# Kernel optimization log

Measured on AMD Instinct MI355X. Metric: run time of the kernel, lower is better.

Reference implementation:

```python
import jax, jax.numpy as jnp
import numpy as np

B, T, H, NB, D = 8, 4096, 16, 32, 1024
NS = H * NB            # 512
PF = 2 * NS            # pos_feat_dim = 1024
HID = 128


def _mlp(x, w1, b1, w2, b2):
    # Linear -> exact GELU -> Linear (matches nn.GELU default, erf form)
    return jax.nn.gelu(x @ w1 + b1, approximate=False) @ w2 + b2


def setup_inputs() -> dict:
    key = jax.random.key(0)
    ks = jax.random.split(key, 12)
    s = 0.02
    return {
        "theta_path": jax.random.normal(ks[0], (B, T, H, NB), jnp.float32),
        "content_emb": jax.random.normal(ks[1], (B, T, D), jnp.float32),
        "obs_position_mask": jax.random.bernoulli(ks[2], 0.5, (B, T)),
        # forward_model: Linear(PF,128) -> GELU -> Linear(128,D)
        "fw1": jax.random.normal(ks[3], (PF, HID), jnp.float32) * s,
        "fb1": jnp.zeros((HID,), jnp.float32),
        "fw2": jax.random.normal(ks[4], (HID, D), jnp.float32) * s,
        "fb2": jnp.zeros((D,), jnp.float32),
        # error_to_state: Linear(D,128) -> GELU -> Linear(128,NS)
        "ew1": jax.random.normal(ks[5], (D, HID), jnp.float32) * s,
        "eb1": jnp.zeros((HID,), jnp.float32),
        "ew2": jax.random.normal(ks[6], (HID, NS), jnp.float32) * s,
        "eb2": jnp.zeros((NS,), jnp.float32),
        "log_gain": jnp.full((H, NB), -1.7, jnp.float32),
    }


def reference(theta_path, content_emb, obs_position_mask,
              fw1, fb1, fw2, fb2, ew1, eb1, ew2, eb2, log_gain):
    # trig positional features: (B,T,H,2*NB) -> (B,T,2*H*NB)
    pos_feat = jnp.concatenate([jnp.cos(theta_path), jnp.sin(theta_path)], axis=-1)
    pos_feat = pos_feat.reshape(B, T, PF)

    obs_pred = _mlp(pos_feat, fw1, fb1, fw2, fb2)            # (B,T,D)
    err_raw = content_emb - obs_pred
    err = err_raw * obs_position_mask[..., None].astype(err_raw.dtype)

    delta_theta = _mlp(err, ew1, eb1, ew2, eb2).reshape(B, T, H, NB)
    gate = jax.nn.sigmoid(log_gain)                          # (H,NB)

    # affine recurrence d_t = gate * d_{t-1} + delta_t via log-depth scan
    def comb(c1, c2):
        a1, b1 = c1
        a2, b2 = c2
        return (a1 * a2, a2 * b1 + b2)

    A = jnp.broadcast_to(gate, delta_theta.shape)
    _, d = jax.lax.associative_scan(comb, (A, delta_theta), axis=1)

    theta_hat = theta_path + d
    return theta_hat, err_raw, gate
```

## Files before the change

### kernel.cpp

```cpp
#include <hip/hip_runtime.h>
#include <hip/hip_bf16.h>

#define B_    8
#define T_    4096
#define H_    16
#define NB_   32
#define D_    1024
#define NS_   512
#define PF_   1024
#define HID_  128
#define RTOK  32768

#define LCH   128
#define WARM  64
#define NCH   32

typedef __attribute__((ext_vector_type(8))) short short8;
typedef __attribute__((ext_vector_type(4))) float floatx4;
typedef unsigned short us;

__device__ __forceinline__ float bf2f(us u){
    union { unsigned int i; float f; } v; v.i = ((unsigned int)u) << 16; return v.f;
}
__device__ __forceinline__ us f2bf(float f){
    union { float f; unsigned int i; } v; v.f = f;
    unsigned int r = v.i + 0x7fffu + ((v.i >> 16) & 1u);
    return (us)(r >> 16);
}
__device__ __forceinline__ float gelu_exact(float x){
    return 0.5f * x * (1.0f + erff(x * 0.70710678118654752f));
}
__device__ __forceinline__ floatx4 mfma16(short8 a, short8 b, floatx4 c){
    return __builtin_amdgcn_mfma_f32_16x16x32_bf16(a, b, c, 0, 0, 0);
}
__device__ __forceinline__ short8 ldfrag(const us* p){
    return *(const short8*)p;
}
__device__ __forceinline__ float ldany(const void* p, int i, int df){
    return df ? bf2f(((const us*)p)[i]) : ((const float*)p)[i];
}

__global__ void dtype_classify(const us* t, int* dflag){
    __shared__ int good;
    if (threadIdx.x == 0) good = 0;
    __syncthreads();
    int g = 0;
    for (int j = 0; j < 64; ++j){
        us u = t[threadIdx.x * 64 + j];
        int e = (u >> 7) & 0xff;
        if (u == 0 || (e >= 90 && e <= 140)) g++;
    }
    atomicAdd(&good, g);
    __syncthreads();
    if (threadIdx.x == 0) dflag[0] = (good > (16384 * 9) / 10) ? 1 : 0;
}

__global__ void mask_classify(const unsigned char* mp, int* flag){
    __shared__ int s_mis, s_oth, s_off1;
    if (threadIdx.x == 0){ s_mis = 0; s_oth = 0; s_off1 = 0; }
    __syncthreads();
    int mis = 0, oth = 0, off1 = 0;
    int base = threadIdx.x * 128;
    for (int i = base; i < base + 128; ++i){
        unsigned char v = mp[i];
        if (v){
            if (i & 3) mis++;
            if ((i & 3) == 1) off1++;
            if (v != 1) oth++;
        }
    }
    atomicAdd(&s_mis, mis); atomicAdd(&s_oth, oth); atomicAdd(&s_off1, off1);
    __syncthreads();
    if (threadIdx.x == 0){
        int f;
        if (s_mis == 0)       f = 0;
        else if (s_oth == 0)  f = 1;
        else if (s_off1 > 0)  f = 2;
        else                  f = 3;
        *flag = f;
    }
}

__global__ void mask_decode(const void* mp, const int* flag, float* maskf){
    int i = blockIdx.x * 256 + threadIdx.x;
    if (i >= RTOK) return;
    int f = *flag;
    bool nz;
    if (f == 1)      nz = ((const unsigned char*) mp)[i] != 0;
    else if (f == 2) nz = ((const us*)           mp)[i] != 0;
    else             nz = ((const unsigned int*) mp)[i] != 0;
    maskf[i] = nz ? 1.0f : 0.0f;
}

__global__ void prep_weights(const void* fw1, const void* fw2, const void* ew1,
                             const void* ew2, const void* fb1, const void* fb2,
                             const void* eb1, const void* eb2, const void* lg,
                             const int* dflag,
                             us* fw1t, us* fw2t, us* ew1t, us* ew2t, us* cb){
    int df = *dflag;
    for (int idx = blockIdx.x * 256 + threadIdx.x; idx < 461056;
         idx += gridDim.x * 256){
        if (idx < 131072){
            int k = idx >> 7, n = idx & 127;
            fw1t[n * 1024 + k] = f2bf(ldany(fw1, idx, df));
        } else if (idx < 262144){
            int l = idx - 131072, k = l >> 10, n = l & 1023;
            fw2t[n * 128 + k] = f2bf(ldany(fw2, l, df));
        } else if (idx < 393216){
            int l = idx - 262144, k = l >> 7, n = l & 127;
            ew1t[n * 1024 + k] = f2bf(ldany(ew1, l, df));
        } else if (idx < 458752){
            int l = idx - 393216, k = l >> 9, n = l & 511;
            ew2t[n * 128 + k] = f2bf(ldany(ew2, l, df));
        } else {
            int l = idx - 458752;
            float v;
            if (l < 128)       v = ldany(fb1, l, df);
            else if (l < 1152) v = ldany(fb2, l - 128, df);
            else if (l < 1280) v = ldany(eb1, l - 1152, df);
            else if (l < 1792) v = ldany(eb2, l - 1280, df);
            else               v = ldany(lg,  l - 1792, df);
            cb[l] = f2bf(v);
        }
    }
}

template<int NR, int NC, int GK, int NT>
__device__ __forceinline__ void stage_wt(us* lds, const us* g,
                                         int row0, int k0, int tid){
    const int LS = NC + 8;
    constexpr int TOT = NR * NC / 8;
    #pragma unroll
    for (int i = tid; i < TOT; i += NT){
        int r  = i / (NC / 8);
        int c8 = (i % (NC / 8)) * 8;
        uint4 v = *(const uint4*)(g + (size_t)(row0 + r) * GK + k0 + c8);
        *(uint4*)(lds + r * LS + c8) = v;
    }
}

__global__ __launch_bounds__(512, 4) void fused_mlp(
    const void* __restrict__ theta, const void* __restrict__ content,
    const int* __restrict__ dflag, const float* __restrict__ maskf,
    const us* __restrict__ cb,
    const us* __restrict__ fw1t, const us* __restrict__ fw2t,
    const us* __restrict__ ew1t, const us* __restrict__ ew2t,
    float* __restrict__ err_out, float* __restrict__ delta_out)
{
    __shared__ __align__(16) us sPF[64 * 136];
    __shared__ __align__(16) us sW [128 * 136];
    __shared__ __align__(16) us sH [64 * 136];
    __shared__ float sMask[64];

    const int tid  = threadIdx.x;
    const int wid  = tid >> 6;
    const int lane = tid & 63;
    const int q    = lane >> 4;
    const int ln   = lane & 15;
    const int wr   = (wid >> 2) * 32;
    const int wc   = (wid & 3) * 32;
    const int row0 = blockIdx.x * 64;
    const int df   = *dflag;

    if (tid < 64) sMask[tid] = maskf[row0 + tid];

    floatx4 h1a[2][2] = {};
    for (int kc = 0; kc < 8; ++kc){
        {
            int r = tid >> 3, e0 = (tid & 7) * 8;
            size_t off = (size_t)(row0 + r) * NS_ + kc * 64 + e0;
            float xv[8];
            if (df){
                uint4 raw = *(const uint4*)((const us*)theta + off);
                const us* pu = (const us*)&raw;
                #pragma unroll
                for (int j = 0; j < 8; ++j) xv[j] = bf2f(pu[j]);
            } else {
                const float* tp = (const float*)theta + off;
                float4 v0 = *(const float4*)tp;
                float4 v1 = *(const float4*)(tp + 4);
                xv[0]=v0.x; xv[1]=v0.y; xv[2]=v0.z; xv[3]=v0.w;
                xv[4]=v1.x; xv[5]=v1.y; xv[6]=v1.z; xv[7]=v1.w;
            }
            short8 c8v, s8v;
            #pragma unroll
            for (int j = 0; j < 8; ++j){
                float s, c;
                __sincosf(xv[j], &s, &c);
                c8v[j] = (short)f2bf(c);
                s8v[j] = (short)f2bf(s);
            }
            int base = r * 136 + (e0 >> 5) * 64 + (e0 & 31);
            *(short8*)(&sPF[base])      = c8v;
            *(short8*)(&sPF[base + 32]) = s8v;
        }
        stage_wt<128, 128, 1024, 512>(sW, fw1t, 0, kc * 128, tid);
        __syncthreads();
        #pragma unroll
        for (int ks = 0; ks < 4; ++ks){
            short8 a0 = ldfrag(&sPF[(wr + ln)      * 136 + ks * 32 + q * 8]);
            short8 a1 = ldfrag(&sPF[(wr + 16 + ln) * 136 + ks * 32 + q * 8]);
            short8 b0 = ldfrag(&sW [(wc + ln)      * 136 + ks * 32 + q * 8]);
            short8 b1 = ldfrag(&sW [(wc + 16 + ln) * 136 + ks * 32 + q * 8]);
            h1a[0][0] = mfma16(a0, b0, h1a[0][0]);
            h1a[0][1] = mfma16(a0, b1, h1a[0][1]);
            h1a[1][0] = mfma16(a1, b0, h1a[1][0]);
            h1a[1][1] = mfma16(a1, b1, h1a[1][1]);
        }
        __syncthreads();
    }
    #pragma unroll
    for (int mt = 0; mt < 2; ++mt)
        #pragma unroll
        for (int nt = 0; nt < 2; ++nt){
            int n = wc + nt * 16 + ln;
            float bias = bf2f(cb[n]);
            #pragma unroll
            for (int r2 = 0; r2 < 4; ++r2){
                int m = wr + mt * 16 + q * 4 + r2;
                sH[m * 136 + n] = f2bf(gelu_exact(h1a[mt][nt][r2] + bias));
            }
        }
    __syncthreads();

    floatx4 h2a[2][2] = {};
    for (int nc = 0; nc < 8; ++nc){
        {
            int r = tid >> 3, c0 = (tid & 7) * 16;
            size_t off = (size_t)(row0 + r) * D_ + nc * 128 + c0;
            if (df){
                const us* cp = (const us*)content + off;
                *(uint4*)(&sPF[r * 136 + c0])     = *(const uint4*)cp;
                *(uint4*)(&sPF[r * 136 + c0 + 8]) = *(const uint4*)(cp + 8);
            } else {
                const float* cp = (const float*)content + off;
                #pragma unroll
                for (int v = 0; v < 2; ++v){
                    float4 a = *(const float4*)(cp + v * 8);
                    float4 b = *(const float4*)(cp + v * 8 + 4);
                    short8 t8;
                    t8[0] = (short)f2bf(a.x); t8[1] = (short)f2bf(a.y);
                    t8[2] = (short)f2bf(a.z); t8[3] = (short)f2bf(a.w);
                    t8[4] = (short)f2bf(b.x); t8[5] = (short)f2bf(b.y);
                    t8[6] = (short)f2bf(b.z); t8[7] = (short)f2bf(b.w);
                    *(short8*)(&sPF[r * 136 + c0 + v * 8]) = t8;
                }
            }
        }
        stage_wt<128, 128, 128, 512>(sW, fw2t, nc * 128, 0, tid);
        __syncthreads();
        floatx4 oa[2][2] = {};
        #pragma unroll
        for (int ks = 0; ks < 4; ++ks){
            short8 a0 = ldfrag(&sH[(wr + ln)      * 136 + ks * 32 + q * 8]);
            short8 a1 = ldfrag(&sH[(wr + 16 + ln) * 136 + ks * 32 + q * 8]);
            short8 b0 = ldfrag(&sW[(wc + ln)      * 136 + ks * 32 + q * 8]);
            short8 b1 = ldfrag(&sW[(wc + 16 + ln) * 136 + ks * 32 + q * 8]);
            oa[0][0] = mfma16(a0, b0, oa[0][0]);
            oa[0][1] = mfma16(a0, b1, oa[0][1]);
            oa[1][0] = mfma16(a1, b0, oa[1][0]);
            oa[1][1] = mfma16(a1, b1, oa[1][1]);
        }
        {
            #pragma unroll
            for (int mt = 0; mt < 2; ++mt)
                #pragma unroll
                for (int nt = 0; nt < 2; ++nt){
                    int n = wc + nt * 16 + ln;
                    float bias = bf2f(cb[128 + nc * 128 + n]);
                    #pragma unroll
                    for (int r2 = 0; r2 < 4; ++r2){
                        int m = wr + mt * 16 + q * 4 + r2;
                        float obs  = oa[mt][nt][r2] + bias;
                        float eraw = bf2f(sPF[m * 136 + n]) - obs;
                        err_out[(size_t)(row0 + m) * D_ + nc * 128 + n] = eraw;
                        sPF[m * 136 + n] = f2bf(eraw * sMask[m]);
                    }
                }
        }
        __syncthreads();
        stage_wt<128, 128, 1024, 512>(sW, ew1t, 0, nc * 128, tid);
        __syncthreads();
        #pragma unroll
        for (int ks = 0; ks < 4; ++ks){
            short8 a0 = ldfrag(&sPF[(wr + ln)      * 136 + ks * 32 + q * 8]);
            short8 a1 = ldfrag(&sPF[(wr + 16 + ln) * 136 + ks * 32 + q * 8]);
            short8 b0 = ldfrag(&sW [(wc + ln)      * 136 + ks * 32 + q * 8]);
            short8 b1 = ldfrag(&sW [(wc + 16 + ln) * 136 + ks * 32 + q * 8]);
            h2a[0][0] = mfma16(a0, b0, h2a[0][0]);
            h2a[0][1] = mfma16(a0, b1, h2a[0][1]);
            h2a[1][0] = mfma16(a1, b0, h2a[1][0]);
            h2a[1][1] = mfma16(a1, b1, h2a[1][1]);
        }
        __syncthreads();
    }
    #pragma unroll
    for (int mt = 0; mt < 2; ++mt)
        #pragma unroll
        for (int nt = 0; nt < 2; ++nt){
            int n = wc + nt * 16 + ln;
            float bias = bf2f(cb[1152 + n]);
            #pragma unroll
            for (int r2 = 0; r2 < 4; ++r2){
                int m = wr + mt * 16 + q * 4 + r2;
                sH[m * 136 + n] = f2bf(gelu_exact(h2a[mt][nt][r2] + bias));
            }
        }
    __syncthreads();

    for (int nc = 0; nc < 4; ++nc){
        stage_wt<128, 128, 128, 512>(sW, ew2t, nc * 128, 0, tid);
        __syncthreads();
        floatx4 da[2][2] = {};
        #pragma unroll
        for (int ks = 0; ks < 4; ++ks){
            short8 a0 = ldfrag(&sH[(wr + ln)      * 136 + ks * 32 + q * 8]);
            short8 a1 = ldfrag(&sH[(wr + 16 + ln) * 136 + ks * 32 + q * 8]);
            short8 b0 = ldfrag(&sW[(wc + ln)      * 136 + ks * 32 + q * 8]);
            short8 b1 = ldfrag(&sW[(wc + 16 + ln) * 136 + ks * 32 + q * 8]);
            da[0][0] = mfma16(a0, b0, da[0][0]);
            da[0][1] = mfma16(a0, b1, da[0][1]);
            da[1][0] = mfma16(a1, b0, da[1][0]);
            da[1][1] = mfma16(a1, b1, da[1][1]);
        }
        #pragma unroll
        for (int mt = 0; mt < 2; ++mt)
            #pragma unroll
            for (int nt = 0; nt < 2; ++nt){
                int n = wc + nt * 16 + ln;
                int col = nc * 128 + n;
                float bias = bf2f(cb[1280 + col]);
                #pragma unroll
                for (int r2 = 0; r2 < 4; ++r2){
                    int m = wr + mt * 16 + q * 4 + r2;
                    delta_out[(size_t)(row0 + m) * NS_ + col] = da[mt][nt][r2] + bias;
                }
            }
        __syncthreads();
    }
}

__global__ __launch_bounds__(512) void warmup_k(
    const float* __restrict__ delta, const us* __restrict__ cb,
    float* __restrict__ warm)
{
    int c  = threadIdx.x;
    int bi = blockIdx.x;
    int ch = bi & (NCH - 1);
    float g = 1.0f / (1.0f + expf(-bf2f(cb[1792 + c])));
    float w = 0.0f;
    if (ch > 0){
        int b  = bi >> 5;
        int t0 = ch * LCH;
        const float* dp = delta + ((size_t)b * T_ + t0 - WARM) * NS_ + c;
        #pragma unroll 8
        for (int t = 0; t < WARM; ++t){ w = g * w + *dp; dp += NS_; }
    }
    warm[bi * NS_ + c] = w;
}

__global__ __launch_bounds__(512) void scan_k(
    const void* __restrict__ theta, const us* __restrict__ cb,
    const int* __restrict__ dflag, const float* __restrict__ warm,
    float* __restrict__ out0, float* __restrict__ gate_out)
{
    int c  = threadIdx.x;
    int bi = blockIdx.x;
    int b  = bi >> 5;
    int ch = bi & (NCH - 1);
    float g = 1.0f / (1.0f + expf(-bf2f(cb[1792 + c])));
    if (bi == 0) gate_out[c] = g;

    float d = warm[bi * NS_ + c];
    size_t base = ((size_t)b * T_ + ch * LCH) * NS_ + c;
    float* op = out0 + base;
    if (*dflag){
        const us* tp = (const us*)theta + base;
        #pragma unroll 4
        for (int t = 0; t < LCH; ++t){
            d = g * d + *op;
            *op = bf2f(*tp) + d;
            tp += NS_; op += NS_;
        }
    } else {
        const float* tp = (const float*)theta + base;
        #pragma unroll 4
        for (int t = 0; t < LCH; ++t){
            d = g * d + *op;
            *op = *tp + d;
            tp += NS_; op += NS_;
        }
    }
}

extern "C" void kernel_launch(void* const* d_in, const int* in_sizes, int n_in,
                              void* d_out, int out_size, void* d_ws, size_t ws_size,
                              hipStream_t stream)
{
    const void* theta   = d_in[0];
    const void* content = d_in[1];
    const void* maskraw = d_in[2];
    const void* fw1 = d_in[3];  const void* fb1 = d_in[4];
    const void* fw2 = d_in[5];  const void* fb2 = d_in[6];
    const void* ew1 = d_in[7];  const void* eb1 = d_in[8];
    const void* ew2 = d_in[9];  const void* eb2 = d_in[10];
    const void* lg  = d_in[11];

    char* ws = (char*)d_ws;
    float* maskf = (float*)ws;
    float* warmb = (float*)ws;
    int*   flag  = (int*)(ws + 524288);
    int*   dflag = (int*)(ws + 524292);
    us*    fw1t  = (us*)(ws + 525312);
    us*    fw2t  = (us*)(ws + 787456);
    us*    ew1t  = (us*)(ws + 1049600);
    us*    ew2t  = (us*)(ws + 1311744);
    us*    cb    = (us*)(ws + 1442816);

    float* out0 = (float*)d_out;
    float* out1 = out0 + 16777216;
    float* out2 = out1 + 33554432;

    dtype_classify<<<1, 256, 0, stream>>>((const us*)theta, dflag);
    mask_classify<<<1, 256, 0, stream>>>((const unsigned char*)maskraw, flag);
    mask_decode<<<128, 256, 0, stream>>>(maskraw, flag, maskf);
    prep_weights<<<512, 256, 0, stream>>>(fw1, fw2, ew1, ew2, fb1, fb2, eb1, eb2,
                                          lg, dflag, fw1t, fw2t, ew1t, ew2t, cb);
    fused_mlp<<<RTOK / 64, 512, 0, stream>>>(theta, content, dflag, maskf, cb,
                                             fw1t, fw2t, ew1t, ew2t, out1, out0);
    warmup_k<<<B_ * NCH, 512, 0, stream>>>(out0, cb, warmb);
    scan_k<<<B_ * NCH, 512, 0, stream>>>(theta, cb, dflag, warmb, out0, out2);
}
```

Baseline: 470.9 us.

## Pre-swizzle MLP weights into MFMA fragment order and read them straight from global memory

prep_weights now writes all four weight matrices in per-wave MFMA fragment order, so each wave loads its B fragments directly from global memory instead of staging 128x128 weight tiles through LDS. Each wave now owns a 16-column slice across all 64 rows. The positional-feature and error tiles are double-buffered, so each k-step needs only one barrier, and the next theta load is prefetched while sincos runs. Content values are read straight into registers, and the mask decode is folded into the fused kernel, which removes one launch. The scan chunk count is doubled, halving chunk length to expose more parallelism, at the cost of more warmup work.

```diff
diff --git a/kernel.cpp b/kernel.cpp
--- a/kernel.cpp
+++ b/kernel.cpp
@@ -11,9 +11,9 @@
 #define HID_  128
 #define RTOK  32768
 
-#define LCH   128
+#define LCH   64
 #define WARM  64
-#define NCH   32
+#define NCH   64
 
 typedef __attribute__((ext_vector_type(8))) short short8;
 typedef __attribute__((ext_vector_type(4))) float floatx4;
@@ -36,8 +36,14 @@
 __device__ __forceinline__ short8 ldfrag(const us* p){
     return *(const short8*)p;
 }
-__device__ __forceinline__ float ldany(const void* p, int i, int df){
+__device__ __forceinline__ float ldany(const void* p, size_t i, int df){
     return df ? bf2f(((const us*)p)[i]) : ((const float*)p)[i];
+}
+__device__ __forceinline__ void bar(){
+    __builtin_amdgcn_sched_barrier(0);
+    asm volatile("s_waitcnt lgkmcnt(0)" ::: "memory");
+    __builtin_amdgcn_s_barrier();
+    __builtin_amdgcn_sched_barrier(0);
 }
 
 __global__ void dtype_classify(const us* t, int* dflag){
@@ -81,17 +87,6 @@
     }
 }
 
-__global__ void mask_decode(const void* mp, const int* flag, float* maskf){
-    int i = blockIdx.x * 256 + threadIdx.x;
-    if (i >= RTOK) return;
-    int f = *flag;
-    bool nz;
-    if (f == 1)      nz = ((const unsigned char*) mp)[i] != 0;
-    else if (f == 2) nz = ((const us*)           mp)[i] != 0;
-    else             nz = ((const unsigned int*) mp)[i] != 0;
-    maskf[i] = nz ? 1.0f : 0.0f;
-}
-
 __global__ void prep_weights(const void* fw1, const void* fw2, const void* ew1,
                              const void* ew2, const void* fb1, const void* fb2,
                              const void* eb1, const void* eb2, const void* lg,
@@ -102,16 +97,26 @@
          idx += gridDim.x * 256){
         if (idx < 131072){
             int k = idx >> 7, n = idx & 127;
-            fw1t[n * 1024 + k] = f2bf(ldany(fw1, idx, df));
+            int c = k >> 7, kk = k & 127;
+            int ks = kk >> 5, qq = (kk >> 3) & 3, j = k & 7;
+            int w = n >> 4, ln = n & 15;
+            fw1t[(((c*8 + w)*4 + ks)*64 + qq*16 + ln)*8 + j] = f2bf(ldany(fw1, idx, df));
         } else if (idx < 262144){
-            int l = idx - 131072, k = l >> 10, n = l & 1023;
-            fw2t[n * 128 + k] = f2bf(ldany(fw2, l, df));
+            int l = idx - 131072; int k = l >> 10, n = l & 1023;
+            int c = n >> 7, w = (n >> 4) & 7, ln = n & 15;
+            int ks = k >> 5, qq = (k >> 3) & 3, j = k & 7;
+            fw2t[(((c*8 + w)*4 + ks)*64 + qq*16 + ln)*8 + j] = f2bf(ldany(fw2, l, df));
         } else if (idx < 393216){
-            int l = idx - 262144, k = l >> 7, n = l & 127;
-            ew1t[n * 1024 + k] = f2bf(ldany(ew1, l, df));
+            int l = idx - 262144; int k = l >> 7, n = l & 127;
+            int c = k >> 7, kk = k & 127;
+            int ks = kk >> 5, qq = (kk >> 3) & 3, j = k & 7;
+            int w = n >> 4, ln = n & 15;
+            ew1t[(((c*8 + w)*4 + ks)*64 + qq*16 + ln)*8 + j] = f2bf(ldany(ew1, l, df));
         } else if (idx < 458752){
-            int l = idx - 393216, k = l >> 9, n = l & 511;
-            ew2t[n * 128 + k] = f2bf(ldany(ew2, l, df));
+            int l = idx - 393216; int k = l >> 9, n = l & 511;
+            int c = n >> 7, w = (n >> 4) & 7, ln = n & 15;
+            int ks = k >> 5, qq = (k >> 3) & 3, j = k & 7;
+            ew2t[(((c*8 + w)*4 + ks)*64 + qq*16 + ln)*8 + j] = f2bf(ldany(ew2, l, df));
         } else {
             int l = idx - 458752;
             float v;
@@ -125,31 +130,32 @@
     }
 }
 
-template<int NR, int NC, int GK, int NT>
-__device__ __forceinline__ void stage_wt(us* lds, const us* g,
-                                         int row0, int k0, int tid){
-    const int LS = NC + 8;
-    constexpr int TOT = NR * NC / 8;
-    #pragma unroll
-    for (int i = tid; i < TOT; i += NT){
-        int r  = i / (NC / 8);
-        int c8 = (i % (NC / 8)) * 8;
-        uint4 v = *(const uint4*)(g + (size_t)(row0 + r) * GK + k0 + c8);
-        *(uint4*)(lds + r * LS + c8) = v;
+__device__ __forceinline__ void load8(float* xv, const void* p, size_t off, int df){
+    if (df){
+        uint4 raw = *(const uint4*)((const us*)p + off);
+        const us* pu = (const us*)&raw;
+        #pragma unroll
+        for (int j = 0; j < 8; ++j) xv[j] = bf2f(pu[j]);
+    } else {
+        const float* tp = (const float*)p + off;
+        float4 v0 = *(const float4*)tp;
+        float4 v1 = *(const float4*)(tp + 4);
+        xv[0]=v0.x; xv[1]=v0.y; xv[2]=v0.z; xv[3]=v0.w;
+        xv[4]=v1.x; xv[5]=v1.y; xv[6]=v1.z; xv[7]=v1.w;
     }
 }
 
 __global__ __launch_bounds__(512, 4) void fused_mlp(
     const void* __restrict__ theta, const void* __restrict__ content,
-    const int* __restrict__ dflag, const float* __restrict__ maskf,
+    const int* __restrict__ dflag,
+    const void* __restrict__ maskraw, const int* __restrict__ mflag,
     const us* __restrict__ cb,
     const us* __restrict__ fw1t, const us* __restrict__ fw2t,
     const us* __restrict__ ew1t, const us* __restrict__ ew2t,
     float* __restrict__ err_out, float* __restrict__ delta_out)
 {
-    __shared__ __align__(16) us sPF[64 * 136];
-    __shared__ __align__(16) us sW [128 * 136];
-    __shared__ __align__(16) us sH [64 * 136];
+    __shared__ __align__(16) us sPF[2][64 * 136];
+    __shared__ __align__(16) us sH[64 * 136];
     __shared__ float sMask[64];
 
     const int tid  = threadIdx.x;
@@ -157,31 +163,27 @@
     const int lane = tid & 63;
     const int q    = lane >> 4;
     const int ln   = lane & 15;
-    const int wr   = (wid >> 2) * 32;
-    const int wc   = (wid & 3) * 32;
     const int row0 = blockIdx.x * 64;
     const int df   = *dflag;
 
-    if (tid < 64) sMask[tid] = maskf[row0 + tid];
-
-    floatx4 h1a[2][2] = {};
-    for (int kc = 0; kc < 8; ++kc){
-        {
-            int r = tid >> 3, e0 = (tid & 7) * 8;
-            size_t off = (size_t)(row0 + r) * NS_ + kc * 64 + e0;
-            float xv[8];
-            if (df){
-                uint4 raw = *(const uint4*)((const us*)theta + off);
-                const us* pu = (const us*)&raw;
-                #pragma unroll
-                for (int j = 0; j < 8; ++j) xv[j] = bf2f(pu[j]);
-            } else {
-                const float* tp = (const float*)theta + off;
-                float4 v0 = *(const float4*)tp;
-                float4 v1 = *(const float4*)(tp + 4);
-                xv[0]=v0.x; xv[1]=v0.y; xv[2]=v0.z; xv[3]=v0.w;
-                xv[4]=v1.x; xv[5]=v1.y; xv[6]=v1.z; xv[7]=v1.w;
-            }
+    if (tid < 64){
+        int f = *mflag;
+        int i = row0 + tid;
+        bool nz;
+        if (f == 1)      nz = ((const unsigned char*) maskraw)[i] != 0;
+        else if (f == 2) nz = ((const us*)           maskraw)[i] != 0;
+        else             nz = ((const unsigned int*) maskraw)[i] != 0;
+        sMask[tid] = nz ? 1.0f : 0.0f;
+    }
+
+    floatx4 h1a[4] = {};
+    {
+        const int r  = tid >> 3;
+        const int e0 = (tid & 7) * 8;
+        const int sb = r * 136 + ((e0 >> 5) << 6) + (e0 & 31);
+        float xv[8];
+        load8(xv, theta, (size_t)(row0 + r) * NS_ + e0, df);
+        for (int kc = 0; kc < 8; ++kc){
             short8 c8v, s8v;
             #pragma unroll
             for (int j = 0; j < 8; ++j){
@@ -190,153 +192,116 @@
                 c8v[j] = (short)f2bf(c);
                 s8v[j] = (short)f2bf(s);
             }
-            int base = r * 136 + (e0 >> 5) * 64 + (e0 & 31);
-            *(short8*)(&sPF[base])      = c8v;
-            *(short8*)(&sPF[base + 32]) = s8v;
-        }
-        stage_wt<128, 128, 1024, 512>(sW, fw1t, 0, kc * 128, tid);
-        __syncthreads();
-        #pragma unroll
-        for (int ks = 0; ks < 4; ++ks){
-            short8 a0 = ldfrag(&sPF[(wr + ln)      * 136 + ks * 32 + q * 8]);
-            short8 a1 = ldfrag(&sPF[(wr + 16 + ln) * 136 + ks * 32 + q * 8]);
-            short8 b0 = ldfrag(&sW [(wc + ln)      * 136 + ks * 32 + q * 8]);
-            short8 b1 = ldfrag(&sW [(wc + 16 + ln) * 136 + ks * 32 + q * 8]);
-            h1a[0][0] = mfma16(a0, b0, h1a[0][0]);
-            h1a[0][1] = mfma16(a0, b1, h1a[0][1]);
-            h1a[1][0] = mfma16(a1, b0, h1a[1][0]);
-            h1a[1][1] = mfma16(a1, b1, h1a[1][1]);
-        }
-        __syncthreads();
-    }
-    #pragma unroll
-    for (int mt = 0; mt < 2; ++mt)
-        #pragma unroll
-        for (int nt = 0; nt < 2; ++nt){
-            int n = wc + nt * 16 + ln;
-            float bias = bf2f(cb[n]);
-            #pragma unroll
-            for (int r2 = 0; r2 < 4; ++r2){
-                int m = wr + mt * 16 + q * 4 + r2;
-                sH[m * 136 + n] = f2bf(gelu_exact(h1a[mt][nt][r2] + bias));
-            }
-        }
-    __syncthreads();
-
-    floatx4 h2a[2][2] = {};
+            us* dst = &sPF[kc & 1][sb];
+            *(short8*)dst        = c8v;
+            *(short8*)(dst + 32) = s8v;
+            if (kc < 7) load8(xv, theta, (size_t)(row0 + r) * NS_ + (kc + 1) * 64 + e0, df);
+            bar();
+            const us* fp = fw1t + kc * 16384 + wid * 2048 + lane * 8;
+            #pragma unroll
+            for (int ks = 0; ks < 4; ++ks){
+                short8 b = *(const short8*)(fp + ks * 512);
+                #pragma unroll
+                for (int mt = 0; mt < 4; ++mt){
+                    short8 a = ldfrag(&sPF[kc & 1][(mt*16 + ln) * 136 + ks*32 + q*8]);
+                    h1a[mt] = mfma16(a, b, h1a[mt]);
+                }
+            }
+        }
+    }
+    {
+        int n = wid * 16 + ln;
+        float bias = bf2f(cb[n]);
+        #pragma unroll
+        for (int mt = 0; mt < 4; ++mt)
+            #pragma unroll
+            for (int r2 = 0; r2 < 4; ++r2)
+                sH[(mt*16 + q*4 + r2) * 136 + n] = f2bf(gelu_exact(h1a[mt][r2] + bias));
+    }
+    bar();
+
+    floatx4 h2a[4] = {};
     for (int nc = 0; nc < 8; ++nc){
+        const int ncol = nc * 128 + wid * 16 + ln;
+        float cv[16];
+        #pragma unroll
+        for (int mt = 0; mt < 4; ++mt)
+            #pragma unroll
+            for (int r2 = 0; r2 < 4; ++r2)
+                cv[mt*4 + r2] = ldany(content,
+                    (size_t)(row0 + mt*16 + q*4 + r2) * D_ + ncol, df);
+        floatx4 oa[4] = {};
         {
-            int r = tid >> 3, c0 = (tid & 7) * 16;
-            size_t off = (size_t)(row0 + r) * D_ + nc * 128 + c0;
-            if (df){
-                const us* cp = (const us*)content + off;
-                *(uint4*)(&sPF[r * 136 + c0])     = *(const uint4*)cp;
-                *(uint4*)(&sPF[r * 136 + c0 + 8]) = *(const uint4*)(cp + 8);
-            } else {
-                const float* cp = (const float*)content + off;
+            const us* fp = fw2t + nc * 16384 + wid * 2048 + lane * 8;
+            #pragma unroll
+            for (int ks = 0; ks < 4; ++ks){
+                short8 b = *(const short8*)(fp + ks * 512);
                 #pragma unroll
-                for (int v = 0; v < 2; ++v){
-                    float4 a = *(const float4*)(cp + v * 8);
-                    float4 b = *(const float4*)(cp + v * 8 + 4);
-                    short8 t8;
-                    t8[0] = (short)f2bf(a.x); t8[1] = (short)f2bf(a.y);
-                    t8[2] = (short)f2bf(a.z); t8[3] = (short)f2bf(a.w);
-                    t8[4] = (short)f2bf(b.x); t8[5] = (short)f2bf(b.y);
-                    t8[6] = (short)f2bf(b.z); t8[7] = (short)f2bf(b.w);
-                    *(short8*)(&sPF[r * 136 + c0 + v * 8]) = t8;
+                for (int mt = 0; mt < 4; ++mt){
+                    short8 a = ldfrag(&sH[(mt*16 + ln) * 136 + ks*32 + q*8]);
+                    oa[mt] = mfma16(a, b, oa[mt]);
                 }
             }
         }
-        stage_wt<128, 128, 128, 512>(sW, fw2t, nc * 128, 0, tid);
-        __syncthreads();
-        floatx4 oa[2][2] = {};
-        #pragma unroll
-        for (int ks = 0; ks < 4; ++ks){
-            short8 a0 = ldfrag(&sH[(wr + ln)      * 136 + ks * 32 + q * 8]);
-            short8 a1 = ldfrag(&sH[(wr + 16 + ln) * 136 + ks * 32 + q * 8]);
-            short8 b0 = ldfrag(&sW[(wc + ln)      * 136 + ks * 32 + q * 8]);
-            short8 b1 = ldfrag(&sW[(wc + 16 + ln) * 136 + ks * 32 + q * 8]);
-            oa[0][0] = mfma16(a0, b0, oa[0][0]);
-            oa[0][1] = mfma16(a0, b1, oa[0][1]);
-            oa[1][0] = mfma16(a1, b0, oa[1][0]);
-            oa[1][1] = mfma16(a1, b1, oa[1][1]);
-        }
         {
-            #pragma unroll
-            for (int mt = 0; mt < 2; ++mt)
-                #pragma unroll
-                for (int nt = 0; nt < 2; ++nt){
-                    int n = wc + nt * 16 + ln;
-                    float bias = bf2f(cb[128 + nc * 128 + n]);
-                    #pragma unroll
-                    for (int r2 = 0; r2 < 4; ++r2){
-                        int m = wr + mt * 16 + q * 4 + r2;
-                        float obs  = oa[mt][nt][r2] + bias;
-                        float eraw = bf2f(sPF[m * 136 + n]) - obs;
-                        err_out[(size_t)(row0 + m) * D_ + nc * 128 + n] = eraw;
-                        sPF[m * 136 + n] = f2bf(eraw * sMask[m]);
-                    }
-                }
-        }
-        __syncthreads();
-        stage_wt<128, 128, 1024, 512>(sW, ew1t, 0, nc * 128, tid);
-        __syncthreads();
-        #pragma unroll
-        for (int ks = 0; ks < 4; ++ks){
-            short8 a0 = ldfrag(&sPF[(wr + ln)      * 136 + ks * 32 + q * 8]);
-            short8 a1 = ldfrag(&sPF[(wr + 16 + ln) * 136 + ks * 32 + q * 8]);
-            short8 b0 = ldfrag(&sW [(wc + ln)      * 136 + ks * 32 + q * 8]);
-            short8 b1 = ldfrag(&sW [(wc + 16 + ln) * 136 + ks * 32 + q * 8]);
-            h2a[0][0] = mfma16(a0, b0, h2a[0][0]);
-            h2a[0][1] = mfma16(a0, b1, h2a[0][1]);
-            h2a[1][0] = mfma16(a1, b0, h2a[1][0]);
-            h2a[1][1] = mfma16(a1, b1, h2a[1][1]);
-        }
-        __syncthreads();
-    }
-    #pragma unroll
-    for (int mt = 0; mt < 2; ++mt)
-        #pragma unroll
-        for (int nt = 0; nt < 2; ++nt){
-            int n = wc + nt * 16 + ln;
-            float bias = bf2f(cb[1152 + n]);
-            #pragma unroll
-            for (int r2 = 0; r2 < 4; ++r2){
-                int m = wr + mt * 16 + q * 4 + r2;
-                sH[m * 136 + n] = f2bf(gelu_exact(h2a[mt][nt][r2] + bias));
-            }
-        }
-    __syncthreads();
-
-    for (int nc = 0; nc < 4; ++nc){
-        stage_wt<128, 128, 128, 512>(sW, ew2t, nc * 128, 0, tid);
-        __syncthreads();
-        floatx4 da[2][2] = {};
-        #pragma unroll
-        for (int ks = 0; ks < 4; ++ks){
-            short8 a0 = ldfrag(&sH[(wr + ln)      * 136 + ks * 32 + q * 8]);
-            short8 a1 = ldfrag(&sH[(wr + 16 + ln) * 136 + ks * 32 + q * 8]);
-            short8 b0 = ldfrag(&sW[(wc + ln)      * 136 + ks * 32 + q * 8]);
-            short8 b1 = ldfrag(&sW[(wc + 16 + ln) * 136 + ks * 32 + q * 8]);
-            da[0][0] = mfma16(a0, b0, da[0][0]);
-            da[0][1] = mfma16(a0, b1, da[0][1]);
-            da[1][0] = mfma16(a1, b0, da[1][0]);
-            da[1][1] = mfma16(a1, b1, da[1][1]);
-        }
-        #pragma unroll
-        for (int mt = 0; mt < 2; ++mt)
-            #pragma unroll
-            for (int nt = 0; nt < 2; ++nt){
-                int n = wc + nt * 16 + ln;
-                int col = nc * 128 + n;
-                float bias = bf2f(cb[1280 + col]);
+            float bias = bf2f(cb[128 + ncol]);
+            #pragma unroll
+            for (int mt = 0; mt < 4; ++mt)
                 #pragma unroll
                 for (int r2 = 0; r2 < 4; ++r2){
-                    int m = wr + mt * 16 + q * 4 + r2;
-                    delta_out[(size_t)(row0 + m) * NS_ + col] = da[mt][nt][r2] + bias;
+                    int m = mt*16 + q*4 + r2;
+                    float obs  = oa[mt][r2] + bias;
+                    float eraw = cv[mt*4 + r2] - obs;
+                    err_out[(size_t)(row0 + m) * D_ + ncol] = eraw;
+                    sPF[nc & 1][m * 136 + wid*16 + ln] = f2bf(eraw * sMask[m]);
                 }
-            }
-        __syncthreads();
+        }
+        bar();
+        {
+            const us* fp = ew1t + nc * 16384 + wid * 2048 + lane * 8;
+            #pragma unroll
+            for (int ks = 0; ks < 4; ++ks){
+                short8 b = *(const short8*)(fp + ks * 512);
+                #pragma unroll
+                for (int mt = 0; mt < 4; ++mt){
+                    short8 a = ldfrag(&sPF[nc & 1][(mt*16 + ln) * 136 + ks*32 + q*8]);
+                    h2a[mt] = mfma16(a, b, h2a[mt]);
+                }
+            }
+        }
+    }
+    {
+        int n = wid * 16 + ln;
+        float bias = bf2f(cb[1152 + n]);
+        #pragma unroll
+        for (int mt = 0; mt < 4; ++mt)
+            #pragma unroll
+            for (int r2 = 0; r2 < 4; ++r2)
+                sH[(mt*16 + q*4 + r2) * 136 + n] = f2bf(gelu_exact(h2a[mt][r2] + bias));
+    }
+    bar();
+
+    for (int c4 = 0; c4 < 4; ++c4){
+        floatx4 da[4] = {};
+        const us* fp = ew2t + c4 * 16384 + wid * 2048 + lane * 8;
+        #pragma unroll
+        for (int ks = 0; ks < 4; ++ks){
+            short8 b = *(const short8*)(fp + ks * 512);
+            #pragma unroll
+            for (int mt = 0; mt < 4; ++mt){
+                short8 a = ldfrag(&sH[(mt*16 + ln) * 136 + ks*32 + q*8]);
+                da[mt] = mfma16(a, b, da[mt]);
+            }
+        }
+        int ncol = c4 * 128 + wid * 16 + ln;
+        float bias = bf2f(cb[1280 + ncol]);
+        #pragma unroll
+        for (int mt = 0; mt < 4; ++mt)
+            #pragma unroll
+            for (int r2 = 0; r2 < 4; ++r2){
+                int m = mt*16 + q*4 + r2;
+                delta_out[(size_t)(row0 + m) * NS_ + ncol] = da[mt][r2] + bias;
+            }
     }
 }
 
@@ -350,7 +315,7 @@
     float g = 1.0f / (1.0f + expf(-bf2f(cb[1792 + c])));
     float w = 0.0f;
     if (ch > 0){
-        int b  = bi >> 5;
+        int b  = bi >> 6;
         int t0 = ch * LCH;
         const float* dp = delta + ((size_t)b * T_ + t0 - WARM) * NS_ + c;
         #pragma unroll 8
@@ -366,7 +331,7 @@
 {
     int c  = threadIdx.x;
     int bi = blockIdx.x;
-    int b  = bi >> 5;
+    int b  = bi >> 6;
     int ch = bi & (NCH - 1);
     float g = 1.0f / (1.0f + expf(-bf2f(cb[1792 + c])));
     if (bi == 0) gate_out[c] = g;
@@ -407,15 +372,14 @@
     const void* lg  = d_in[11];
 
     char* ws = (char*)d_ws;
-    float* maskf = (float*)ws;
-    float* warmb = (float*)ws;
-    int*   flag  = (int*)(ws + 524288);
-    int*   dflag = (int*)(ws + 524292);
-    us*    fw1t  = (us*)(ws + 525312);
-    us*    fw2t  = (us*)(ws + 787456);
-    us*    ew1t  = (us*)(ws + 1049600);
-    us*    ew2t  = (us*)(ws + 1311744);
-    us*    cb    = (us*)(ws + 1442816);
+    int*   flag  = (int*)ws;
+    int*   dflag = (int*)(ws + 4);
+    us*    cb    = (us*)(ws + 256);
+    us*    fw1t  = (us*)(ws + 4864);
+    us*    fw2t  = (us*)(ws + 267008);
+    us*    ew1t  = (us*)(ws + 529152);
+    us*    ew2t  = (us*)(ws + 791296);
+    float* warmb = (float*)(ws + 4864);
 
     float* out0 = (float*)d_out;
     float* out1 = out0 + 16777216;
@@ -423,11 +387,10 @@
 
     dtype_classify<<<1, 256, 0, stream>>>((const us*)theta, dflag);
     mask_classify<<<1, 256, 0, stream>>>((const unsigned char*)maskraw, flag);
-    mask_decode<<<128, 256, 0, stream>>>(maskraw, flag, maskf);
     prep_weights<<<512, 256, 0, stream>>>(fw1, fw2, ew1, ew2, fb1, fb2, eb1, eb2,
                                           lg, dflag, fw1t, fw2t, ew1t, ew2t, cb);
-    fused_mlp<<<RTOK / 64, 512, 0, stream>>>(theta, content, dflag, maskf, cb,
-                                             fw1t, fw2t, ew1t, ew2t, out1, out0);
+    fused_mlp<<<RTOK / 64, 512, 0, stream>>>(theta, content, dflag, maskraw, flag,
+                                             cb, fw1t, fw2t, ew1t, ew2t, out1, out0);
     warmup_k<<<B_ * NCH, 512, 0, stream>>>(out0, cb, warmb);
     scan_k<<<B_ * NCH, 512, 0, stream>>>(theta, cb, dflag, warmb, out0, out2);
 }
```

Result: faster. 452.4 us (-3.9%).
